# Kernel optimization log

Hardware: AMD Instinct MI355X
Metric: run time of the kernel (lower is better)

Reference implementation:

```python
import jax, jax.numpy as jnp
import numpy as np

B = 16384   # batch
S = 512     # state_size
A = 512     # action_size
H = 1024    # hidden_dim
L = 64      # latent_size
E = 6       # num_experts
G = 32      # gate hidden size
IN = S + L      # first-layer input size
INT = H + L     # intermediate input size
SIGMA = 0.05


def setup_inputs() -> dict:
    key = jax.random.key(0)
    ks = jax.random.split(key, 20)

    def u(k, shape, s):
        return jax.random.uniform(k, shape, jnp.float32, -s, s)

    inp = {}
    inp['state'] = jax.random.normal(ks[0], (B, S), jnp.float32)
    inp['latent'] = jax.random.normal(ks[1], (B, L), jnp.float32)
    # expert decoder layers: (E, J, K) weights, (E, K) biases; torch init: w ~ U(-3/sqrt(J), 3/sqrt(J)), b ~ U(-1/sqrt(J), 1/sqrt(J))
    dims = [(IN, H), (INT, H), (INT, H), (INT, A)]
    for i, (j, k_) in enumerate(dims):
        stdv = 1.0 / np.sqrt(j)
        inp[f'w{i}'] = u(ks[2 + 2 * i], (E, j, k_), 3.0 * stdv)
        inp[f'b{i}'] = u(ks[3 + 2 * i], (E, k_), stdv)
    # gating MLP: IN -> G -> G -> E
    gdims = [(IN, G), (G, G), (G, E)]
    for i, (a, b) in enumerate(gdims):
        s = 1.0 / np.sqrt(a)
        inp[f'gw{i}'] = u(ks[10 + 2 * i], (a, b), s)
        inp[f'gb{i}'] = u(ks[11 + 2 * i], (b,), s)
    return inp


def reference(state, latent, w0, b0, w1, b1, w2, b2, w3, b3,
              gw0, gb0, gw1, gb1, gw2, gb2):
    xc = jnp.concatenate([state, latent], axis=-1)          # [B, IN]
    # gating MLP with ELU activations, softmax over experts
    h = jax.nn.elu(xc @ gw0 + gb0)
    h = jax.nn.elu(h @ gw1 + gb1)
    coef = jax.nn.softmax(h @ gw2 + gb2, axis=-1)           # [B, E]

    layer_out = state
    ws = [w0, w1, w2, w3]
    bs = [b0, b1, b2, b3]
    for i in range(4):
        inp = jnp.concatenate([layer_out, latent], axis=-1)  # [B, J]
        # per-sample soft-mixed expert matmul + bias
        mixed = jnp.einsum('be,bj,ejk->bk', coef, inp, ws[i],
                           optimize=True) + coef @ bs[i]      # [B, K]
        layer_out = jax.nn.elu(mixed) if i < 3 else mixed

    # reparameterize with fixed sigma: mu + eps * sigma (eps from a fixed key for determinism)
    eps = jax.random.normal(jax.random.key(42), layer_out.shape, layer_out.dtype)
    return layer_out + eps * SIGMA
```

## Files before the change

kernel.cpp:

```cpp
#include <hip/hip_runtime.h>

typedef _Float16 f16;
typedef _Float16 half8 __attribute__((ext_vector_type(8)));
typedef float f32x4 __attribute__((ext_vector_type(4)));
typedef unsigned int u32;

#define B_    16384
#define E_    6
#define ASTR  1088
#define AOUT  512

__device__ __forceinline__ u32 swz(u32 row, u32 ch) {
  return row * 128u + ((ch ^ (row & 7u)) * 16u);
}

__device__ __forceinline__ float elu_f(float x) {
  return x > 0.f ? x : (__expf(x) - 1.f);
}

__device__ __forceinline__ half8 splat8(f16 s) {
  half8 v = {s, s, s, s, s, s, s, s};
  return v;
}

__device__ __forceinline__ void gload16(const f16* g, char* l) {
  __builtin_amdgcn_global_load_lds(
      (const __attribute__((address_space(1))) void*)g,
      (__attribute__((address_space(3))) void*)l, 16, 0, 0);
}

__device__ __forceinline__ float jax_eps(u32 idx) {
  const u32 k0 = 0u, k1 = 42u;
  const u32 k2 = k0 ^ k1 ^ 0x1BD11BDAu;
  u32 x0 = 0u + k0, x1 = idx + k1;
#define TFR(r) { x0 += x1; x1 = (x1 << (r)) | (x1 >> (32 - (r))); x1 ^= x0; }
  TFR(13) TFR(15) TFR(26) TFR(6)   x0 += k1; x1 += k2 + 1u;
  TFR(17) TFR(29) TFR(16) TFR(24)  x0 += k2; x1 += k0 + 2u;
  TFR(13) TFR(15) TFR(26) TFR(6)   x0 += k0; x1 += k1 + 3u;
  TFR(17) TFR(29) TFR(16) TFR(24)  x0 += k1; x1 += k2 + 4u;
  TFR(13) TFR(15) TFR(26) TFR(6)   x0 += k2; x1 += k0 + 5u;
#undef TFR
  u32 bits = x0 ^ x1;
  float f = __uint_as_float(0x3f800000u | (bits >> 9)) - 1.0f;
  const float lo = -0.99999994f;
  float u = fmaxf(lo, fmaf(f, 2.0f, lo));
  float w = -__logf(fmaf(-u, u, 1.0f));
  float p;
  if (w < 5.0f) {
    w -= 2.5f;
    p = 2.81022636e-08f;
    p = fmaf(p, w, 3.43273939e-07f);
    p = fmaf(p, w, -3.5233877e-06f);
    p = fmaf(p, w, -4.39150654e-06f);
    p = fmaf(p, w, 0.00021858087f);
    p = fmaf(p, w, -0.00125372503f);
    p = fmaf(p, w, -0.00417768164f);
    p = fmaf(p, w, 0.246640727f);
    p = fmaf(p, w, 1.50140941f);
  } else {
    w = __fsqrt_rn(w) - 3.0f;
    p = -0.000200214257f;
    p = fmaf(p, w, 0.000100950558f);
    p = fmaf(p, w, 0.00134934322f);
    p = fmaf(p, w, -0.00367342844f);
    p = fmaf(p, w, 0.00573950773f);
    p = fmaf(p, w, -0.0076224613f);
    p = fmaf(p, w, 0.00943887047f);
    p = fmaf(p, w, 1.00167406f);
    p = fmaf(p, w, 2.83297682f);
  }
  return 1.41421356f * p * u;
}

__global__ void prep_act(const float* __restrict__ state, const float* __restrict__ latent,
                         f16* __restrict__ actA, f16* __restrict__ actB) {
  const u32 NS = (B_ * 512u) / 8u;
  const u32 NL = (B_ * 64u) / 8u;
  u32 i = blockIdx.x * 256u + threadIdx.x;
  if (i < NS) {
    u32 e = i * 8u;
    u32 b = e >> 9, c = e & 511u;
    float4 v0 = *(const float4*)(state + e);
    float4 v1 = *(const float4*)(state + e + 4);
    half8 h;
    h[0]=(f16)v0.x; h[1]=(f16)v0.y; h[2]=(f16)v0.z; h[3]=(f16)v0.w;
    h[4]=(f16)v1.x; h[5]=(f16)v1.y; h[6]=(f16)v1.z; h[7]=(f16)v1.w;
    *(half8*)(actA + (size_t)b * ASTR + c) = h;
  } else if (i < NS + NL) {
    u32 e = (i - NS) * 8u;
    u32 b = e >> 6, c = e & 63u;
    float4 v0 = *(const float4*)(latent + e);
    float4 v1 = *(const float4*)(latent + e + 4);
    half8 h;
    h[0]=(f16)v0.x; h[1]=(f16)v0.y; h[2]=(f16)v0.z; h[3]=(f16)v0.w;
    h[4]=(f16)v1.x; h[5]=(f16)v1.y; h[6]=(f16)v1.z; h[7]=(f16)v1.w;
    *(half8*)(actA + (size_t)b * ASTR + 512 + c) = h;
    *(half8*)(actA + (size_t)b * ASTR + 1024 + c) = h;
    *(half8*)(actB + (size_t)b * ASTR + 1024 + c) = h;
  }
}

__global__ void prep_gw0(const float* __restrict__ gw0, f16* __restrict__ g0hi,
                         f16* __restrict__ g0lo) {
  int i = blockIdx.x * 256 + threadIdx.x;
  if (i < 32 * 576) {
    int n = i / 576, j = i % 576;
    float v = gw0[j * 32 + n];
    f16 h = (f16)v;
    g0hi[i] = h;
    g0lo[i] = (f16)(v - (float)h);
  }
}

__global__ void transpose_w(const float* __restrict__ w, f16* __restrict__ wt,
                            int J, int K) {
  __shared__ float t[64][65];
  int tiles_j = J >> 6, tiles_k = K >> 6;
  int per_e = tiles_j * tiles_k;
  int bid = blockIdx.x;
  int e = bid / per_e, rem = bid % per_e;
  int jt = rem / tiles_k, kt = rem % tiles_k;
  int tid = threadIdx.x;
  int r = tid >> 2, c0 = (tid & 3) << 4;
  const float* src = w + ((size_t)e * J + (size_t)jt * 64 + r) * K + (size_t)kt * 64 + c0;
  float4 v0 = *(const float4*)(src);
  float4 v1 = *(const float4*)(src + 4);
  float4 v2 = *(const float4*)(src + 8);
  float4 v3 = *(const float4*)(src + 12);
  t[r][c0+0]=v0.x;  t[r][c0+1]=v0.y;  t[r][c0+2]=v0.z;  t[r][c0+3]=v0.w;
  t[r][c0+4]=v1.x;  t[r][c0+5]=v1.y;  t[r][c0+6]=v1.z;  t[r][c0+7]=v1.w;
  t[r][c0+8]=v2.x;  t[r][c0+9]=v2.y;  t[r][c0+10]=v2.z; t[r][c0+11]=v2.w;
  t[r][c0+12]=v3.x; t[r][c0+13]=v3.y; t[r][c0+14]=v3.z; t[r][c0+15]=v3.w;
  __syncthreads();
  int kr = tid >> 2, jq = (tid & 3) << 4;
  half8 p0, p1;
#pragma unroll
  for (int m = 0; m < 8; m++) {
    p0[m] = (f16)t[jq + m][kr];
    p1[m] = (f16)t[jq + 8 + m][kr];
  }
  f16* dst = wt + ((size_t)e * K + (size_t)kt * 64 + kr) * J + (size_t)jt * 64 + jq;
  *(half8*)(dst) = p0;
  *(half8*)(dst + 8) = p1;
}

__global__ __launch_bounds__(256) void gating_kernel(
    const float* __restrict__ state, const float* __restrict__ latent,
    const f16* __restrict__ g0hi, const f16* __restrict__ g0lo,
    const float* __restrict__ gb0, const float* __restrict__ gw1,
    const float* __restrict__ gb1, const float* __restrict__ gw2,
    const float* __restrict__ gb2, float* __restrict__ coefT) {
  __shared__ __align__(16) char sm[24576];
  __shared__ float h_lds[64][33];
  char* Ahi = sm;
  char* Alo = sm + 8192;
  char* Bhi = sm + 16384;
  char* Blo = sm + 20480;
  const int tid = threadIdx.x, lane = tid & 63, wave = tid >> 6;
  const int b0 = blockIdx.x * 64;

  f32x4 acc[2];
#pragma unroll
  for (int n = 0; n < 2; n++) {
    float v = gb0[n * 16 + (lane & 15)];
    f32x4 t = {v, v, v, v};
    acc[n] = t;
  }

  for (int kt = 0; kt < 9; ++kt) {
    __syncthreads();
    int r = tid >> 2, cq = (tid & 3) << 4;
    float xv[16];
    if (kt < 8) {
      const float* s = state + (size_t)(b0 + r) * 512 + kt * 64 + cq;
      *(float4*)(xv)      = *(const float4*)(s);
      *(float4*)(xv + 4)  = *(const float4*)(s + 4);
      *(float4*)(xv + 8)  = *(const float4*)(s + 8);
      *(float4*)(xv + 12) = *(const float4*)(s + 12);
    } else {
      const float* s = latent + (size_t)(b0 + r) * 64 + cq;
      *(float4*)(xv)      = *(const float4*)(s);
      *(float4*)(xv + 4)  = *(const float4*)(s + 4);
      *(float4*)(xv + 8)  = *(const float4*)(s + 8);
      *(float4*)(xv + 12) = *(const float4*)(s + 12);
    }
    half8 hh[2], hl[2];
#pragma unroll
    for (int q = 0; q < 2; q++)
#pragma unroll
      for (int i = 0; i < 8; i++) {
        float x = xv[q * 8 + i];
        f16 h = (f16)x;
        hh[q][i] = h;
        hl[q][i] = (f16)(x - (float)h);
      }
    *(half8*)(Ahi + swz(r, (tid & 3) * 2 + 0)) = hh[0];
    *(half8*)(Ahi + swz(r, (tid & 3) * 2 + 1)) = hh[1];
    *(half8*)(Alo + swz(r, (tid & 3) * 2 + 0)) = hl[0];
    *(half8*)(Alo + swz(r, (tid & 3) * 2 + 1)) = hl[1];
    int nb = tid >> 3, chb = tid & 7;
    half8 bh = *(const half8*)(g0hi + (size_t)nb * 576 + kt * 64 + chb * 8);
    half8 bl = *(const half8*)(g0lo + (size_t)nb * 576 + kt * 64 + chb * 8);
    *(half8*)(Bhi + swz(nb, chb)) = bh;
    *(half8*)(Blo + swz(nb, chb)) = bl;
    __syncthreads();
#pragma unroll
    for (int ks = 0; ks < 2; ks++) {
      int arow = wave * 16 + (lane & 15);
      int ch = ks * 4 + (lane >> 4);
      half8 ah = *(const half8*)(Ahi + swz(arow, ch));
      half8 al = *(const half8*)(Alo + swz(arow, ch));
#pragma unroll
      for (int n = 0; n < 2; n++) {
        int brow = n * 16 + (lane & 15);
        half8 wh = *(const half8*)(Bhi + swz(brow, ch));
        half8 wl = *(const half8*)(Blo + swz(brow, ch));
        acc[n] = __builtin_amdgcn_mfma_f32_16x16x32_f16(ah, wh, acc[n], 0, 0, 0);
        acc[n] = __builtin_amdgcn_mfma_f32_16x16x32_f16(al, wh, acc[n], 0, 0, 0);
        acc[n] = __builtin_amdgcn_mfma_f32_16x16x32_f16(ah, wl, acc[n], 0, 0, 0);
      }
    }
  }
#pragma unroll
  for (int n = 0; n < 2; n++)
#pragma unroll
    for (int i = 0; i < 4; i++) {
      int row = wave * 16 + (lane >> 4) * 4 + i;
      int col = n * 16 + (lane & 15);
      h_lds[row][col] = elu_f(acc[n][i]);
    }
  __syncthreads();
  {
    int row = tid & 63, q = tid >> 6;
    float a2[8];
#pragma unroll
    for (int o = 0; o < 8; o++) a2[o] = gb1[q * 8 + o];
    for (int j = 0; j < 32; j++) {
      float v = h_lds[row][j];
#pragma unroll
      for (int o = 0; o < 8; o++) a2[o] = fmaf(v, gw1[j * 32 + q * 8 + o], a2[o]);
    }
    __syncthreads();
#pragma unroll
    for (int o = 0; o < 8; o++) h_lds[row][q * 8 + o] = elu_f(a2[o]);
  }
  __syncthreads();
  if (wave == 0) {
    float lg[6];
#pragma unroll
    for (int e = 0; e < 6; e++) lg[e] = gb2[e];
    for (int j = 0; j < 32; j++) {
      float v = h_lds[lane][j];
#pragma unroll
      for (int e = 0; e < 6; e++) lg[e] = fmaf(v, gw2[j * 6 + e], lg[e]);
    }
    float mx = lg[0];
#pragma unroll
    for (int e = 1; e < 6; e++) mx = fmaxf(mx, lg[e]);
    float s = 0.f, pc[6];
#pragma unroll
    for (int e = 0; e < 6; e++) { pc[e] = __expf(lg[e] - mx); s += pc[e]; }
    float inv = 1.0f / s;
#pragma unroll
    for (int e = 0; e < 6; e++) coefT[e * B_ + b0 + lane] = pc[e] * inv;
  }
}

template <int J, int KOUT, int MODE>
__global__ __launch_bounds__(256, 2) void moe_gemm(
    const f16* __restrict__ act, const f16* __restrict__ wt,
    const float* __restrict__ coefT, const float* __restrict__ bias,
    f16* __restrict__ out_act, float* __restrict__ out_f32) {
  constexpr int NSUB = J / 64;
  constexpr int NTILE = KOUT / 128;
  __shared__ __align__(16) char sm[49152];
  char* As  = sm;
  char* Bs0 = sm + 16384;
  char* Bs1 = sm + 32768;

  const int tid = threadIdx.x;
  const int lane = tid & 63;
  const int wv = tid >> 6;
  const int wr = wv >> 1, wc = wv & 1;
  const int nwg = gridDim.x;
  const int cpx = nwg >> 3;
  const int bid = (blockIdx.x & 7) * cpx + (blockIdx.x >> 3);
  const int b0 = (bid / NTILE) * 128;
  const int n0 = (bid % NTILE) * 128;

  int srow[4], scol[4];
#pragma unroll
  for (int i = 0; i < 4; i++) {
    int r = wv * 32 + i * 8 + (lane >> 3);
    srow[i] = r;
    scol[i] = ((lane & 7) ^ (r & 7)) * 8;
  }

  auto stageA = [&](int ks) {
#pragma unroll
    for (int i = 0; i < 4; i++)
      gload16(act + (size_t)(b0 + srow[i]) * ASTR + ks * 64 + scol[i],
              As + (wv * 4 + i) * 1024);
  };
  auto stageB = [&](int e, int ks, char* Bs) {
    const f16* wb = wt + (size_t)e * KOUT * J;
#pragma unroll
    for (int i = 0; i < 4; i++)
      gload16(wb + (size_t)(n0 + srow[i]) * J + ks * 64 + scol[i],
              Bs + (wv * 4 + i) * 1024);
  };

  stageA(0);
  stageB(0, 0, Bs0);

  f16 cfh[E_][4];
#pragma unroll
  for (int e = 0; e < E_; e++)
#pragma unroll
    for (int m = 0; m < 4; m++)
      cfh[e][m] = (f16)coefT[e * B_ + b0 + wr * 64 + m * 16 + (lane & 15)];

  f32x4 acc[4][4];
#pragma unroll
  for (int m = 0; m < 4; m++)
#pragma unroll
    for (int n = 0; n < 4; n++) {
      f32x4 z = {0.f, 0.f, 0.f, 0.f};
      acc[m][n] = z;
    }
#pragma unroll
  for (int e = 0; e < E_; e++) {
    float bv[4];
#pragma unroll
    for (int n = 0; n < 4; n++)
      bv[n] = bias[e * KOUT + n0 + wc * 64 + n * 16 + (lane & 15)];
#pragma unroll
    for (int m = 0; m < 4; m++)
#pragma unroll
      for (int i = 0; i < 4; i++) {
        float cv = coefT[e * B_ + b0 + wr * 64 + m * 16 + (lane >> 4) * 4 + i];
#pragma unroll
        for (int n = 0; n < 4; n++) acc[m][n][i] = fmaf(cv, bv[n], acc[m][n][i]);
      }
  }

  half8 afr[2][4];

  for (int ks = 0; ks < NSUB; ++ks) {
#pragma unroll
    for (int e = 0; e < E_; ++e) {
      __syncthreads();
      char* Bcur = (e & 1) ? Bs1 : Bs0;
      char* Bnxt = (e & 1) ? Bs0 : Bs1;
      if (e < E_ - 1) {
        stageB(e + 1, ks, Bnxt);
      } else if (ks + 1 < NSUB) {
        stageB(0, ks + 1, Bnxt);
        stageA(ks + 1);
      }
      if (e == 0) {
#pragma unroll
        for (int h = 0; h < 2; h++)
#pragma unroll
          for (int m = 0; m < 4; m++) {
            int row = wr * 64 + m * 16 + (lane & 15);
            afr[h][m] = *(const half8*)(As + swz(row, h * 4 + (lane >> 4)));
          }
      }
#pragma unroll
      for (int h = 0; h < 2; h++) {
        half8 bf[4], afs[4];
#pragma unroll
        for (int n = 0; n < 4; n++) {
          int rn = wc * 64 + n * 16 + (lane & 15);
          bf[n] = *(const half8*)(Bcur + swz(rn, h * 4 + (lane >> 4)));
        }
#pragma unroll
        for (int m = 0; m < 4; m++) afs[m] = afr[h][m] * splat8(cfh[e][m]);
#pragma unroll
        for (int m = 0; m < 4; m++)
#pragma unroll
          for (int n = 0; n < 4; n++)
            acc[m][n] = __builtin_amdgcn_mfma_f32_16x16x32_f16(afs[m], bf[n], acc[m][n], 0, 0, 0);
      }
    }
  }
#pragma unroll
  for (int m = 0; m < 4; m++)
#pragma unroll
    for (int n = 0; n < 4; n++)
#pragma unroll
      for (int i = 0; i < 4; i++) {
        int row = b0 + wr * 64 + m * 16 + (lane >> 4) * 4 + i;
        int col = n0 + wc * 64 + n * 16 + (lane & 15);
        float x = acc[m][n][i];
        if (MODE == 0) {
          out_act[(size_t)row * ASTR + col] = (f16)elu_f(x);
        } else {
          u32 idx = (u32)row * AOUT + col;
          out_f32[idx] = fmaf(0.05f, jax_eps(idx), x);
        }
      }
}

extern "C" void kernel_launch(void* const* d_in, const int* in_sizes, int n_in,
                              void* d_out, int out_size, void* d_ws, size_t ws_size,
                              hipStream_t stream) {
  (void)in_sizes; (void)n_in; (void)out_size; (void)ws_size;
  const float* state  = (const float*)d_in[0];
  const float* latent = (const float*)d_in[1];
  const float* w0 = (const float*)d_in[2];
  const float* b0 = (const float*)d_in[3];
  const float* w1 = (const float*)d_in[4];
  const float* b1 = (const float*)d_in[5];
  const float* w2 = (const float*)d_in[6];
  const float* b2 = (const float*)d_in[7];
  const float* w3 = (const float*)d_in[8];
  const float* b3 = (const float*)d_in[9];
  const float* gw0 = (const float*)d_in[10];
  const float* gb0 = (const float*)d_in[11];
  const float* gw1 = (const float*)d_in[12];
  const float* gb1 = (const float*)d_in[13];
  const float* gw2 = (const float*)d_in[14];
  const float* gb2 = (const float*)d_in[15];

  char* ws = (char*)d_ws;
  size_t off = 0;
  float* coefT = (float*)(ws + off); off += (size_t)E_ * B_ * 4;
  f16* actA = (f16*)(ws + off); off += (size_t)B_ * ASTR * 2;
  f16* actB = (f16*)(ws + off); off += (size_t)B_ * ASTR * 2;
  f16* wt0 = (f16*)(ws + off); off += (size_t)E_ * 1024 * 576 * 2;
  f16* wt1 = (f16*)(ws + off); off += (size_t)E_ * 1024 * 1088 * 2;
  f16* wt2 = (f16*)(ws + off); off += (size_t)E_ * 1024 * 1088 * 2;
  f16* wt3 = (f16*)(ws + off); off += (size_t)E_ * 512 * 1088 * 2;
  f16* g0hi = (f16*)(ws + off); off += 32 * 576 * 2;
  f16* g0lo = (f16*)(ws + off); off += 32 * 576 * 2;

  prep_act<<<4608, 256, 0, stream>>>(state, latent, actA, actB);
  prep_gw0<<<72, 256, 0, stream>>>(gw0, g0hi, g0lo);
  transpose_w<<<6 * 9 * 16, 256, 0, stream>>>(w0, wt0, 576, 1024);
  transpose_w<<<6 * 17 * 16, 256, 0, stream>>>(w1, wt1, 1088, 1024);
  transpose_w<<<6 * 17 * 16, 256, 0, stream>>>(w2, wt2, 1088, 1024);
  transpose_w<<<6 * 17 * 8, 256, 0, stream>>>(w3, wt3, 1088, 512);
  gating_kernel<<<256, 256, 0, stream>>>(state, latent, g0hi, g0lo, gb0, gw1, gb1,
                                         gw2, gb2, coefT);
  moe_gemm<576, 1024, 0><<<1024, 256, 0, stream>>>(actA, wt0, coefT, b0, actB, nullptr);
  moe_gemm<1088, 1024, 0><<<1024, 256, 0, stream>>>(actB, wt1, coefT, b1, actA, nullptr);
  moe_gemm<1088, 1024, 0><<<1024, 256, 0, stream>>>(actA, wt2, coefT, b2, actB, nullptr);
  moe_gemm<1088, 512, 1><<<512, 256, 0, stream>>>(actB, wt3, coefT, b3, nullptr, (float*)d_out);
}
```

Measured before the change: 738.0 us.

## Triple-buffer expert weight tiles with prefetch depth two and explicit vmcnt waits

Shared memory grows to 64KB so expert weight tiles can rotate through three buffers, with loads issued two expert steps ahead instead of one. The generic __syncthreads (which drains all outstanding loads) is replaced by partial s_waitcnt vmcnt plus s_barrier, and the activation-tile prefetch moves to the second expert step. The goal is to keep more global-to-LDS traffic in flight and stop each step from waiting on every pending load. MFMA blocks are also wrapped in s_setprio. The trade-off is more LDS per block, which may limit occupancy, and the hand-tuned wait counts must match the number of issued loads exactly.

```diff
diff --git a/kernel.cpp b/kernel.cpp
--- a/kernel.cpp
+++ b/kernel.cpp
@@ -28,6 +28,8 @@
       (const __attribute__((address_space(1))) void*)g,
       (__attribute__((address_space(3))) void*)l, 16, 0, 0);
 }
+
+#define WAITVM(N) asm volatile("s_waitcnt vmcnt(" #N ")" ::: "memory")
 
 __device__ __forceinline__ float jax_eps(u32 idx) {
   const u32 k0 = 0u, k1 = 42u;
@@ -273,10 +275,7 @@
     f16* __restrict__ out_act, float* __restrict__ out_f32) {
   constexpr int NSUB = J / 64;
   constexpr int NTILE = KOUT / 128;
-  __shared__ __align__(16) char sm[49152];
-  char* As  = sm;
-  char* Bs0 = sm + 16384;
-  char* Bs1 = sm + 32768;
+  __shared__ __align__(16) char sm[65536];
 
   const int tid = threadIdx.x;
   const int lane = tid & 63;
@@ -296,14 +295,17 @@
     scol[i] = ((lane & 7) ^ (r & 7)) * 8;
   }
 
+  char* const As = sm;
+
   auto stageA = [&](int ks) {
 #pragma unroll
     for (int i = 0; i < 4; i++)
       gload16(act + (size_t)(b0 + srow[i]) * ASTR + ks * 64 + scol[i],
               As + (wv * 4 + i) * 1024);
   };
-  auto stageB = [&](int e, int ks, char* Bs) {
+  auto stageB = [&](int e, int ks, int buf) {
     const f16* wb = wt + (size_t)e * KOUT * J;
+    char* Bs = sm + 16384 + buf * 16384;
 #pragma unroll
     for (int i = 0; i < 4; i++)
       gload16(wb + (size_t)(n0 + srow[i]) * J + ks * 64 + scol[i],
@@ -311,7 +313,8 @@
   };
 
   stageA(0);
-  stageB(0, 0, Bs0);
+  stageB(0, 0, 0);
+  stageB(1, 0, 1);
 
   f16 cfh[E_][4];
 #pragma unroll
@@ -346,45 +349,58 @@
 
   half8 afr[2][4];
 
-  for (int ks = 0; ks < NSUB; ++ks) {
-#pragma unroll
-    for (int e = 0; e < E_; ++e) {
-      __syncthreads();
-      char* Bcur = (e & 1) ? Bs1 : Bs0;
-      char* Bnxt = (e & 1) ? Bs0 : Bs1;
-      if (e < E_ - 1) {
-        stageB(e + 1, ks, Bnxt);
-      } else if (ks + 1 < NSUB) {
-        stageB(0, ks + 1, Bnxt);
-        stageA(ks + 1);
+  auto compute = [&](int buf, int e, bool loadA) {
+    char* Bcur = sm + 16384 + buf * 16384;
+    if (loadA) {
+#pragma unroll
+      for (int h = 0; h < 2; h++)
+#pragma unroll
+        for (int m = 0; m < 4; m++) {
+          int row = wr * 64 + m * 16 + (lane & 15);
+          afr[h][m] = *(const half8*)(As + swz(row, h * 4 + (lane >> 4)));
+        }
+    }
+#pragma unroll
+    for (int h = 0; h < 2; h++) {
+      half8 bf[4], afs[4];
+#pragma unroll
+      for (int n = 0; n < 4; n++) {
+        int rn = wc * 64 + n * 16 + (lane & 15);
+        bf[n] = *(const half8*)(Bcur + swz(rn, h * 4 + (lane >> 4)));
       }
-      if (e == 0) {
-#pragma unroll
-        for (int h = 0; h < 2; h++)
-#pragma unroll
-          for (int m = 0; m < 4; m++) {
-            int row = wr * 64 + m * 16 + (lane & 15);
-            afr[h][m] = *(const half8*)(As + swz(row, h * 4 + (lane >> 4)));
-          }
-      }
-#pragma unroll
-      for (int h = 0; h < 2; h++) {
-        half8 bf[4], afs[4];
-#pragma unroll
-        for (int n = 0; n < 4; n++) {
-          int rn = wc * 64 + n * 16 + (lane & 15);
-          bf[n] = *(const half8*)(Bcur + swz(rn, h * 4 + (lane >> 4)));
-        }
-#pragma unroll
-        for (int m = 0; m < 4; m++) afs[m] = afr[h][m] * splat8(cfh[e][m]);
-#pragma unroll
-        for (int m = 0; m < 4; m++)
-#pragma unroll
-          for (int n = 0; n < 4; n++)
-            acc[m][n] = __builtin_amdgcn_mfma_f32_16x16x32_f16(afs[m], bf[n], acc[m][n], 0, 0, 0);
-      }
-    }
-  }
+#pragma unroll
+      for (int m = 0; m < 4; m++) afs[m] = afr[h][m] * splat8(cfh[e][m]);
+      __builtin_amdgcn_s_setprio(1);
+#pragma unroll
+      for (int m = 0; m < 4; m++)
+#pragma unroll
+        for (int n = 0; n < 4; n++)
+          acc[m][n] = __builtin_amdgcn_mfma_f32_16x16x32_f16(afs[m], bf[n], acc[m][n], 0, 0, 0);
+      __builtin_amdgcn_s_setprio(0);
+    }
+  };
+
+  for (int ks = 0; ks < NSUB - 1; ++ks) {
+#pragma unroll
+    for (int e = 0; e < 6; ++e) {
+      if (e == 2 || e == 3) { WAITVM(8); } else { WAITVM(4); }
+      __builtin_amdgcn_s_barrier();
+      stageB((e + 2) % 6, ks + (e + 2) / 6, (e + 2) % 3);
+      if (e == 1) stageA(ks + 1);
+      compute(e % 3, e, e == 0);
+    }
+  }
+  {
+    const int ks = NSUB - 1;
+#pragma unroll
+    for (int e = 0; e < 6; ++e) {
+      if (e == 5) { WAITVM(0); } else { WAITVM(4); }
+      __builtin_amdgcn_s_barrier();
+      if (e <= 3) stageB(e + 2, ks, (e + 2) % 3);
+      compute(e % 3, e, e == 0);
+    }
+  }
+
 #pragma unroll
   for (int m = 0; m < 4; m++)
 #pragma unroll
```

New measurement: 732.8 us. Within noise of the previous version (-0.7%).
